# Performance work log

Measured on AMD Instinct MI355X. Metric: run time of the kernel, lower is better.

## Reference

```python
import jax, jax.numpy as jnp
import numpy as np
import math

HIDDEN = 256
INPUT_SIZE = 32

def setup_inputs() -> dict:
    key = jax.random.key(0)
    k1, k2, k3 = jax.random.split(key, 3)
    stdv = 1.0 / math.sqrt(HIDDEN)
    inp = jax.random.normal(k1, (32, 48, 24, INPUT_SIZE), dtype=jnp.float32)
    W = jax.random.uniform(k2, (6 * HIDDEN, INPUT_SIZE + 2 * HIDDEN), minval=-stdv, maxval=stdv, dtype=jnp.float32)
    Bp = jax.random.uniform(k3, (6 * HIDDEN,), minval=-stdv, maxval=stdv, dtype=jnp.float32)
    return {"input": inp, "W": W, "Bp": Bp}

def _witran_forward(input, W, Bp):
    B, rows, cols, C = input.shape
    H = W.shape[0] // 6
    # flag == 1: permute to (cols, batch, rows, C)
    x = jnp.transpose(input, (2, 0, 1, 3))
    R = cols            # Water2sea_slice_num
    Lorig = rows        # Original_slice_len
    L = R + Lorig - 1   # Water2sea_slice_len
    # input_transfer: row r occupies slice positions r : r+Lorig (pad then roll)
    padded = jnp.pad(x, ((0, 0), (0, 0), (0, R - 1), (0, 0)))        # (R, B, L, C)
    shifted = jax.vmap(lambda xr, r: jnp.roll(xr, r, axis=1))(padded, jnp.arange(R))
    a = shifted.reshape(R * B, L, C)
    a_slices = jnp.transpose(a, (1, 0, 2))                            # (L, R*B, C)
    r_idx = jnp.repeat(jnp.arange(R), B)                              # (R*B,)

    def step(carry, inp):
        h_row, h_col = carry
        s, xs = inp
        # bias applied only to first (s+1)*B rows and only while s < R (faithful to torch)
        mask = ((r_idx <= s) & (s < R)).astype(xs.dtype)[:, None]
        gate = jnp.concatenate([h_row, h_col, xs], axis=-1) @ W.T + mask * Bp
        sig = jax.nn.sigmoid(gate[:, : 4 * H])
        tg = jnp.tanh(gate[:, 4 * H:])
        u_row, o_row, u_col, o_col = jnp.split(sig, 4, axis=-1)
        i_row, i_col = jnp.split(tg, 2, axis=-1)
        h_row = jnp.tanh((1.0 - u_row) * h_row + u_row * i_row) * o_row
        h_col_new = jnp.tanh((1.0 - u_col) * h_col + u_col * i_col) * o_col
        # roll col hidden down by one batch block for next diagonal
        h_col_rolled = jnp.roll(h_col_new, B, axis=0)
        return (h_row, h_col_rolled), (h_row, h_col_new)

    init = (jnp.zeros((R * B, H), input.dtype), jnp.zeros((R * B, H), input.dtype))
    _, (rows_all, cols_all) = jax.lax.scan(step, init, (jnp.arange(L), a_slices))
    # output_all_slice: stack along slice dim -> (R*B, L, 2H)
    output_all = jnp.transpose(jnp.concatenate([rows_all, cols_all], axis=-1), (1, 0, 2))
    rows_r = rows_all.reshape(L, R, B, H)
    cols_r = cols_all.reshape(L, R, B, H)
    # row hidden saved at slice s = Lorig-1+k from block k (diagonal)
    hidden_row = rows_r[jnp.arange(Lorig - 1, L), jnp.arange(R)]      # (R, B, H)
    # col hidden saved at slices s >= R-1 from the last block (pre-roll)
    hidden_col = cols_r[R - 1:, R - 1]                                # (Lorig, B, H)
    hidden_row_all = jnp.transpose(hidden_row, (1, 0, 2)).reshape(B, 1, R, H)
    hidden_col_all = jnp.transpose(hidden_col, (1, 0, 2)).reshape(B, 1, Lorig, H)
    # flag == 1 return order: (output, hidden_col_all, hidden_row_all)
    return output_all, hidden_col_all, hidden_row_all

def reference(input, W, Bp):
    return _witran_forward(input, W, Bp)
```

## Files before the change

### kernel.cpp

```cpp
#include <hip/hip_runtime.h>
#include <cstddef>


namespace {
constexpr int H_   = 256;
constexpr int R_   = 24;
constexpr int LOR_ = 48;
constexpr int L_   = 71;
constexpr int N_   = 768;
constexpr int KH_  = 512;
constexpr int KT_  = 544;
constexpr int AST_ = 552;
}

typedef __attribute__((ext_vector_type(8))) _Float16       f16x8;
typedef __attribute__((ext_vector_type(8))) unsigned short u16x8;
typedef __attribute__((ext_vector_type(4))) float          f32x4;

__device__ __forceinline__ float fsig(float x)  { return 1.f / (1.f + __expf(-x)); }
__device__ __forceinline__ float ftanhf(float x){ float e = __expf(2.f * x); return 1.f - 2.f / (e + 1.f); }

__global__ __launch_bounds__(256) void prep_all(const float* __restrict__ W,
                                                const float* __restrict__ inp,
                                                _Float16* __restrict__ Wfrag,
                                                _Float16* __restrict__ xall,
                                                unsigned long long* __restrict__ zb) {
    const int bx = blockIdx.x;
    const int t  = threadIdx.x;
    if (bx < 3264) {
        int o = bx * 256 + t;
        int j8   = o & 7;
        int lane = (o >> 3) & 63;
        int rest = o >> 9;
        int lt   = rest % 96;
        int kc   = rest / 96;
        int n0 = lane & 15, quad = lane >> 4;
        int lg  = lt * 16 + n0;
        int kt  = lg / 96;
        int rem = lg % 96;
        int g  = rem >> 4, kl = rem & 15;
        int j  = g * 256 + kt * 16 + kl;
        int kg = kc * 32 + quad * 8 + j8;
        Wfrag[o] = (_Float16)W[j * KT_ + kg];
    } else if (bx < 10080) {
        int o = (bx - 3264) * 256 + t;
        int c = o & 31;
        int n = (o >> 5) % N_;
        int s = (o >> 5) / N_;
        int r = n >> 5, b = n & 31;
        int l = s - r;
        float v = 0.f;
        if (l >= 0 && l < LOR_) v = inp[((b * LOR_ + l) * R_ + r) * 32 + c];
        xall[o] = (_Float16)v;
    } else {
        zb[(bx - 10080) * 256 + t] = 0ull;
    }
}

__global__ __launch_bounds__(768, 3) void step_k(
    const _Float16* __restrict__ Wfrag,
    const _Float16* __restrict__ xall,
    const _Float16* __restrict__ hbc,
    _Float16*       __restrict__ hbn,
    const float* __restrict__ Bp,
    float* __restrict__ out0, float* __restrict__ out1, float* __restrict__ out2,
    int s)
{
    __shared__ unsigned short As[48 * AST_];
    __shared__ float Gt[2][48][98];

    const int t    = threadIdx.x;
    const int wv   = t >> 6;
    const int lane = t & 63;
    const int n0   = lane & 15;
    const int quad = lane >> 4;

    int kt, mc;
    if (s >= 22) {
        int x = blockIdx.x & 7, q = blockIdx.x >> 3;
        kt = q & 15; mc = ((q >> 4) << 3) | x;
    } else {
        kt = blockIdx.x & 15; mc = blockIdx.x >> 4;
    }

    const bool hi = (wv >= 6);
    const int  g  = hi ? wv - 6 : wv;

    f16x8 bfr[9];
    f16x8 xf[3];
    if (!hi) {
#pragma unroll
        for (int i = 0; i < 9; ++i)
            bfr[i] = *(const f16x8*)(const void*)(
                Wfrag + ((size_t)(i * 96 + kt * 6 + g) * 64 + lane) * 8);
    } else {
#pragma unroll
        for (int i = 0; i < 8; ++i)
            bfr[i] = *(const f16x8*)(const void*)(
                Wfrag + ((size_t)((9 + i) * 96 + kt * 6 + g) * 64 + lane) * 8);
#pragma unroll
        for (int mt = 0; mt < 3; ++mt)
            xf[mt] = *(const f16x8*)(const void*)(
                xall + ((size_t)(s * N_ + mc * 48 + mt * 16 + n0)) * 32 + quad * 8);
    }

    const int mm = t >> 4;
    const int kp = t & 15;
    const int n  = mc * 48 + mm;
    const int k  = kt * 16 + kp;
    float bp[6];
    if (s < R_) {
#pragma unroll
        for (int gg = 0; gg < 6; ++gg)
            bp[gg] = Bp[gg * 256 + k];
    }

#pragma unroll
    for (int it = 0; it < 4; ++it) {
        int q   = it * 768 + t;
        int row = q >> 6;
        int col = (q & 63) * 8;
        *(u16x8*)(void*)(&As[row * AST_ + col]) =
            *(const u16x8*)(const void*)((const unsigned short*)hbc +
                                         (size_t)(mc * 48 + row) * KH_ + col);
    }
    __syncthreads();

    f32x4 acc[3];
#pragma unroll
    for (int mt = 0; mt < 3; ++mt) acc[mt] = (f32x4){0.f, 0.f, 0.f, 0.f};

    if (!hi) {
#pragma unroll
        for (int i = 0; i < 9; ++i) {
            f16x8 a[3];
#pragma unroll
            for (int mt = 0; mt < 3; ++mt)
                a[mt] = *(const f16x8*)(const void*)(
                    &As[(mt * 16 + n0) * AST_ + i * 32 + quad * 8]);
#pragma unroll
            for (int mt = 0; mt < 3; ++mt)
                acc[mt] = __builtin_amdgcn_mfma_f32_16x16x32_f16(a[mt], bfr[i], acc[mt], 0, 0, 0);
        }
    } else {
#pragma unroll
        for (int i = 0; i < 7; ++i) {
            f16x8 a[3];
#pragma unroll
            for (int mt = 0; mt < 3; ++mt)
                a[mt] = *(const f16x8*)(const void*)(
                    &As[(mt * 16 + n0) * AST_ + (9 + i) * 32 + quad * 8]);
#pragma unroll
            for (int mt = 0; mt < 3; ++mt)
                acc[mt] = __builtin_amdgcn_mfma_f32_16x16x32_f16(a[mt], bfr[i], acc[mt], 0, 0, 0);
        }
#pragma unroll
        for (int mt = 0; mt < 3; ++mt)
            acc[mt] = __builtin_amdgcn_mfma_f32_16x16x32_f16(xf[mt], bfr[7], acc[mt], 0, 0, 0);
    }

    {
        float (*gt)[98] = Gt[hi ? 1 : 0];
#pragma unroll
        for (int mt = 0; mt < 3; ++mt)
#pragma unroll
            for (int reg = 0; reg < 4; ++reg)
                gt[mt * 16 + quad * 4 + reg][g * 16 + n0] = acc[mt][reg];
    }
    __syncthreads();

    {
        const int r  = n >> 5, b = n & 31;
        const bool useb = (r <= s) && (s < R_);

        float gv[6];
#pragma unroll
        for (int gg = 0; gg < 6; ++gg) {
            float v = Gt[0][mm][gg * 16 + kp] + Gt[1][mm][gg * 16 + kp];
            gv[gg] = useb ? (v + bp[gg]) : v;
        }

        float hro = (float)*(const _Float16*)(const void*)&As[mm * AST_ + k];
        float hco = (float)*(const _Float16*)(const void*)&As[mm * AST_ + 256 + k];

        float ur = fsig(gv[0]), oR = fsig(gv[1]);
        float uc = fsig(gv[2]), oc = fsig(gv[3]);
        float ir = ftanhf(gv[4]), ic = ftanhf(gv[5]);
        float hrv = ftanhf((1.f - ur) * hro + ur * ir) * oR;
        float hcv = ftanhf((1.f - uc) * hco + uc * ic) * oc;

        float* o0 = out0 + ((size_t)n * L_ + s) * 512;
        __builtin_nontemporal_store(hrv, o0 + k);
        __builtin_nontemporal_store(hcv, o0 + 256 + k);

        int n2 = n + 32; if (n2 >= N_) n2 -= N_;
        hbn[(size_t)n  * KH_ + k]       = (_Float16)hrv;
        hbn[(size_t)n2 * KH_ + 256 + k] = (_Float16)hcv;

        if (s >= LOR_ - 1 && r == s - (LOR_ - 1))
            __builtin_nontemporal_store(hrv, out2 + (size_t)(b * R_ + r) * H_ + k);
        if (r == R_ - 1 && s >= R_ - 1)
            __builtin_nontemporal_store(hcv, out1 + (size_t)(b * LOR_ + (s - (R_ - 1))) * H_ + k);
    }
}

extern "C" void kernel_launch(void* const* d_in, const int* in_sizes, int n_in,
                              void* d_out, int out_size, void* d_ws, size_t ws_size,
                              hipStream_t stream) {
    const float* inp = (const float*)d_in[0];
    const float* W   = (const float*)d_in[1];
    const float* Bp  = (const float*)d_in[2];

    float* out0 = (float*)d_out;
    float* out1 = out0 + (size_t)N_ * L_ * 512;
    float* out2 = out1 + (size_t)32 * LOR_ * H_;

    char* ws = (char*)d_ws;
    _Float16* Wfrag = (_Float16*)(ws);
    _Float16* xall  = (_Float16*)(ws + 1671168);
    _Float16* hb0   = (_Float16*)(ws + 5160960);
    _Float16* hb1   = (_Float16*)(ws + 5947392);

    prep_all<<<10848, 256, 0, stream>>>(W, inp, Wfrag, xall,
                                        (unsigned long long*)hb0);

    for (int s = 0; s < L_; ++s) {
        const _Float16* hbc = (s & 1) ? hb1 : hb0;
        _Float16*       hbn = (s & 1) ? hb0 : hb1;
        int act = (s < 23 ? s : 23) + 1;
        int nmc = (32 * act + 47) / 48;
        step_k<<<nmc * 16, 768, 0, stream>>>(Wfrag, xall, hbc, hbn,
                                             Bp, out0, out1, out2, s);
    }
}
```

Baseline: 579.1 us.

## Read input directly in step kernel, drop xall prep, remap block order

Removes the precomputed fp16 xall buffer, so the prep kernel no longer gathers and converts the full padded input for every slice. Each step kernel now loads its input rows directly from the fp32 input and converts them in registers. The change also repads the Gt shared buffer stride to 112 and reorders the block-to-(kt,mc) mapping for the later steps, to change the LDS bank pattern and how blocks land on the hardware. The trade-off is strided fp32 gathers inside the latency-critical per-step kernel in exchange for a smaller prep kernel and less workspace traffic.

After: 655.5 us. 13.2% more time.

```diff
diff --git a/kernel.cpp b/kernel.cpp
--- a/kernel.cpp
+++ b/kernel.cpp
@@ -11,6 +11,7 @@
 constexpr int KH_  = 512;
 constexpr int KT_  = 544;
 constexpr int AST_ = 552;
+constexpr int GST_ = 112;
 }
 
 typedef __attribute__((ext_vector_type(8))) _Float16       f16x8;
@@ -21,9 +22,7 @@
 __device__ __forceinline__ float ftanhf(float x){ float e = __expf(2.f * x); return 1.f - 2.f / (e + 1.f); }
 
 __global__ __launch_bounds__(256) void prep_all(const float* __restrict__ W,
-                                                const float* __restrict__ inp,
                                                 _Float16* __restrict__ Wfrag,
-                                                _Float16* __restrict__ xall,
                                                 unsigned long long* __restrict__ zb) {
     const int bx = blockIdx.x;
     const int t  = threadIdx.x;
@@ -42,24 +41,14 @@
         int j  = g * 256 + kt * 16 + kl;
         int kg = kc * 32 + quad * 8 + j8;
         Wfrag[o] = (_Float16)W[j * KT_ + kg];
-    } else if (bx < 10080) {
-        int o = (bx - 3264) * 256 + t;
-        int c = o & 31;
-        int n = (o >> 5) % N_;
-        int s = (o >> 5) / N_;
-        int r = n >> 5, b = n & 31;
-        int l = s - r;
-        float v = 0.f;
-        if (l >= 0 && l < LOR_) v = inp[((b * LOR_ + l) * R_ + r) * 32 + c];
-        xall[o] = (_Float16)v;
-    } else {
-        zb[(bx - 10080) * 256 + t] = 0ull;
+    } else {
+        zb[(bx - 3264) * 256 + t] = 0ull;
     }
 }
 
 __global__ __launch_bounds__(768, 3) void step_k(
     const _Float16* __restrict__ Wfrag,
-    const _Float16* __restrict__ xall,
+    const float*    __restrict__ inp,
     const _Float16* __restrict__ hbc,
     _Float16*       __restrict__ hbn,
     const float* __restrict__ Bp,
@@ -67,7 +56,7 @@
     int s)
 {
     __shared__ unsigned short As[48 * AST_];
-    __shared__ float Gt[2][48][98];
+    __shared__ float Gt[2][48][GST_];
 
     const int t    = threadIdx.x;
     const int wv   = t >> 6;
@@ -77,8 +66,9 @@
 
     int kt, mc;
     if (s >= 22) {
-        int x = blockIdx.x & 7, q = blockIdx.x >> 3;
-        kt = q & 15; mc = ((q >> 4) << 3) | x;
+        int x = blockIdx.x & 7;
+        mc = (x << 1) | ((blockIdx.x >> 3) & 1);
+        kt = blockIdx.x >> 4;
     } else {
         kt = blockIdx.x & 15; mc = blockIdx.x >> 4;
     }
@@ -99,9 +89,22 @@
             bfr[i] = *(const f16x8*)(const void*)(
                 Wfrag + ((size_t)((9 + i) * 96 + kt * 6 + g) * 64 + lane) * 8);
 #pragma unroll
-        for (int mt = 0; mt < 3; ++mt)
-            xf[mt] = *(const f16x8*)(const void*)(
-                xall + ((size_t)(s * N_ + mc * 48 + mt * 16 + n0)) * 32 + quad * 8);
+        for (int mt = 0; mt < 3; ++mt) {
+            int n = mc * 48 + mt * 16 + n0;
+            int r = n >> 5, b = n & 31;
+            int l = s - r;
+            if (l >= 0 && l < LOR_) {
+                const float* xp = inp + (((size_t)b * LOR_ + l) * R_ + r) * 32 + quad * 8;
+                f32x4 lo = *(const f32x4*)(const void*)(xp);
+                f32x4 hh = *(const f32x4*)(const void*)(xp + 4);
+                f16x8 v;
+#pragma unroll
+                for (int j = 0; j < 4; ++j) { v[j] = (_Float16)lo[j]; v[4 + j] = (_Float16)hh[j]; }
+                xf[mt] = v;
+            } else {
+                xf[mt] = (f16x8){0, 0, 0, 0, 0, 0, 0, 0};
+            }
+        }
     }
 
     const int mm = t >> 4;
@@ -160,7 +163,7 @@
     }
 
     {
-        float (*gt)[98] = Gt[hi ? 1 : 0];
+        float (*gt)[GST_] = Gt[hi ? 1 : 0];
 #pragma unroll
         for (int mt = 0; mt < 3; ++mt)
 #pragma unroll
@@ -217,19 +220,17 @@
 
     char* ws = (char*)d_ws;
     _Float16* Wfrag = (_Float16*)(ws);
-    _Float16* xall  = (_Float16*)(ws + 1671168);
-    _Float16* hb0   = (_Float16*)(ws + 5160960);
-    _Float16* hb1   = (_Float16*)(ws + 5947392);
-
-    prep_all<<<10848, 256, 0, stream>>>(W, inp, Wfrag, xall,
-                                        (unsigned long long*)hb0);
+    _Float16* hb0   = (_Float16*)(ws + 1671168);
+    _Float16* hb1   = (_Float16*)(ws + 2457600);
+
+    prep_all<<<4032, 256, 0, stream>>>(W, Wfrag, (unsigned long long*)hb0);
 
     for (int s = 0; s < L_; ++s) {
         const _Float16* hbc = (s & 1) ? hb1 : hb0;
         _Float16*       hbn = (s & 1) ? hb0 : hb1;
         int act = (s < 23 ? s : 23) + 1;
         int nmc = (32 * act + 47) / 48;
-        step_k<<<nmc * 16, 768, 0, stream>>>(Wfrag, xall, hbc, hbn,
+        step_k<<<nmc * 16, 768, 0, stream>>>(Wfrag, inp, hbc, hbn,
                                              Bp, out0, out1, out2, s);
     }
 }
```
